# Kernel optimization log

Measured on AMD Instinct MI355X. Metric: run time of the kernel, lower is better.

## Reference

```python
import jax, jax.numpy as jnp
import numpy as np
from jax.scipy.special import logsumexp

B, N, V = 16, 25, 10000
WDIM, HDIM, ZDIM, SD = 512, 512, 64, 256
T, NT = 60, 30
S = NT + T          # all_states
NEG = -1e9          # log-zero surrogate (keeps grads finite)


def setup_inputs() -> dict:
    key = jax.random.key(0)
    ks = jax.random.split(key, 32)
    g = lambda k, shape, s=0.02: (jax.random.normal(k, shape) * s).astype(jnp.float32)
    z4 = lambda *shape: jnp.zeros(shape, jnp.float32)
    return {
        "x": jax.random.randint(ks[0], (B, N), 0, V),
        "eps": jax.random.normal(ks[1], (B, ZDIM), dtype=jnp.float32),
        "enc_emb": g(ks[2], (V, WDIM), 0.1),
        "lstm_f_wih": g(ks[3], (WDIM, 4 * HDIM)),
        "lstm_f_whh": g(ks[4], (HDIM, 4 * HDIM)),
        "lstm_f_b": z4(4 * HDIM),
        "lstm_b_wih": g(ks[5], (WDIM, 4 * HDIM)),
        "lstm_b_whh": g(ks[6], (HDIM, 4 * HDIM)),
        "lstm_b_b": z4(4 * HDIM),
        "encp_w": g(ks[7], (2 * HDIM, 2 * ZDIM)),
        "encp_b": z4(2 * ZDIM),
        "t_emb": g(ks[8], (T, SD), 1.0),
        "nt_emb": g(ks[9], (NT, SD), 1.0),
        "root_emb": g(ks[10], (1, SD), 1.0),
        "rule_w": g(ks[11], (SD + ZDIM, S * S)),
        "rule_b": z4(S * S),
        "root_w1": g(ks[12], (SD + ZDIM, SD)),
        "root_b1": z4(SD),
        "root_resw": g(ks[13], (4, SD, SD)),
        "root_resb": z4(4, SD),
        "root_w2": g(ks[14], (SD, NT)),
        "root_b2": z4(NT),
        "voc_w1": g(ks[15], (SD + ZDIM, SD)),
        "voc_b1": z4(SD),
        "voc_resw": g(ks[16], (4, SD, SD)),
        "voc_resb": z4(4, SD),
        "voc_w2": g(ks[17], (SD, V)),
        "voc_b2": z4(V),
    }


def _mlp(h0, w1, b1, resw, resb, w2, b2):
    h = h0 @ w1 + b1
    for i in range(2):
        a = jax.nn.relu(h @ resw[2 * i] + resb[2 * i])
        h = jax.nn.relu(a @ resw[2 * i + 1] + resb[2 * i + 1]) + h
    return h @ w2 + b2


def _lstm(emb_tbw, wih, whh, b):
    # emb_tbw: [time, batch, w_dim] -> hidden states [time, batch, H]
    H = whh.shape[0]
    Bsz = emb_tbw.shape[1]

    def step(carry, xt):
        h, c = carry
        gates = xt @ wih + h @ whh + b
        i, f, gg, o = jnp.split(gates, 4, axis=-1)
        c = jax.nn.sigmoid(f) * c + jax.nn.sigmoid(i) * jnp.tanh(gg)
        h = jax.nn.sigmoid(o) * jnp.tanh(c)
        return (h, c), h

    init = (jnp.zeros((Bsz, H), emb_tbw.dtype), jnp.zeros((Bsz, H), emb_tbw.dtype))
    _, hs = jax.lax.scan(step, init, emb_tbw)
    return hs


def _inside(unary, rule, root):
    # unary: [B,n,T] preterminal scores; rule: [B,NT,S,S]; root: [B,NT]
    Bsz, n, _ = unary.shape
    chart = jnp.full((Bsz, n, n, S), NEG, unary.dtype)
    ar = jnp.arange(n)
    chart = chart.at[:, ar, ar, NT:].set(unary)  # width-1 spans = terminals
    for w in range(2, n + 1):
        ii = jnp.arange(n - w + 1)          # span starts
        u = jnp.arange(1, w)                # split offsets
        left = chart[:, ii[:, None], ii[:, None] + u[None, :] - 1, :]    # [B,ns,w-1,S]
        right = chart[:, ii[:, None] + u[None, :], ii[:, None] + w - 1, :]
        # lse over split points, then over (B,C) children against rules
        m2 = logsumexp(left[..., :, None] + right[..., None, :], axis=2)  # [B,ns,S,S]
        score = logsumexp(rule[:, None] + m2[:, :, None], axis=(-2, -1))  # [B,ns,NT]
        chart = chart.at[:, ii, ii + w - 1, :NT].set(score)
    return logsumexp(root + chart[:, 0, n - 1, :NT], axis=-1)  # [B]


def reference(x, eps, enc_emb, lstm_f_wih, lstm_f_whh, lstm_f_b,
              lstm_b_wih, lstm_b_whh, lstm_b_b, encp_w, encp_b,
              t_emb, nt_emb, root_emb, rule_w, rule_b,
              root_w1, root_b1, root_resw, root_resb, root_w2, root_b2,
              voc_w1, voc_b1, voc_resw, voc_resb, voc_w2, voc_b2):
    # --- variational encoder ---
    emb_t = jnp.swapaxes(enc_emb[x], 0, 1)                      # [N,B,W]
    hf = _lstm(emb_t, lstm_f_wih, lstm_f_whh, lstm_f_b)
    hb = _lstm(emb_t[::-1], lstm_b_wih, lstm_b_whh, lstm_b_b)[::-1]
    h = jnp.concatenate([hf, hb], axis=-1).max(axis=0)          # [B,2H] max over time
    params = h @ encp_w + encp_b
    mean, logvar = params[:, :ZDIM], params[:, ZDIM:]
    kl = (-0.5 * (logvar - mean ** 2 - jnp.exp(logvar) + 1.0)).sum(1)
    z = jnp.exp(0.5 * logvar) * eps + mean                       # [B,z]
    # --- root scores ---
    root_in = jnp.concatenate([jnp.broadcast_to(root_emb, (B, SD)), z], 1)
    root_scores = jax.nn.log_softmax(
        _mlp(root_in, root_w1, root_b1, root_resw, root_resb, root_w2, root_b2), axis=1)
    # --- unary scores (score each preterminal once, gather per token) ---
    t_in = jnp.concatenate([jnp.broadcast_to(t_emb[None], (B, T, SD)),
                            jnp.broadcast_to(z[:, None], (B, T, ZDIM))], -1)
    vocab_scores = jax.nn.log_softmax(
        _mlp(t_in, voc_w1, voc_b1, voc_resw, voc_resb, voc_w2, voc_b2), axis=-1)  # [B,T,V]
    unary = vocab_scores[jnp.arange(B)[:, None], :, x]           # [B,N,T]
    # --- binary rule scores ---
    nt_in = jnp.concatenate([jnp.broadcast_to(nt_emb[None], (B, NT, SD)),
                             jnp.broadcast_to(z[:, None], (B, NT, ZDIM))], -1)
    rule_scores = jax.nn.log_softmax(nt_in @ rule_w + rule_b, axis=-1).reshape(B, NT, S, S)
    # --- inside algorithm ---
    log_Z = _inside(unary, rule_scores, root_scores)
    return -log_Z, kl
```

## Files before the change

### kernel.cpp

```cpp
#include <hip/hip_runtime.h>
#include <hip/hip_bf16.h>
#include <math.h>

#define BB 16
#define NN 25
#define VV 10000
#define WD 512
#define HD 512
#define ZD 64
#define SDIM 256
#define TT 60
#define NTS 30
#define SSYM 90
#define S2 8100
#define NEGV -1000000000.0f

__global__ void k_emb(const int* __restrict__ x, const float* __restrict__ enc_emb,
                      float* __restrict__ emb) {
    int i = blockIdx.x * 256 + threadIdx.x;
    if (i >= 400 * 512) return;
    int r = i >> 9, k = i & 511;
    emb[i] = enc_emb[(size_t)x[r] * 512 + k];
}

__global__ __launch_bounds__(256) void gemm_f32(const float* __restrict__ A,
    const float* __restrict__ Bm, const float* __restrict__ bias,
    const float* __restrict__ res, float* __restrict__ C,
    int M, int Nn, int K, int do_relu)
{
    __shared__ float As[16][65];
    __shared__ float Bs[16][65];
    int tid = threadIdx.x;
    int tx = tid & 15, ty = tid >> 4;
    int bm = blockIdx.y * 64, bn = blockIdx.x * 64;
    float acc[4][4] = {};
    for (int k0 = 0; k0 < K; k0 += 16) {
#pragma unroll
        for (int l = 0; l < 4; ++l) {
            int idx = tid * 4 + l;
            int kk = idx & 15, mm = idx >> 4;
            int gr = bm + mm;
            As[kk][mm] = (gr < M) ? A[(size_t)gr * K + (k0 + kk)] : 0.f;
            int kb = idx >> 6, nn = idx & 63;
            int gc = bn + nn;
            Bs[kb][nn] = (gc < Nn) ? Bm[(size_t)(k0 + kb) * Nn + gc] : 0.f;
        }
        __syncthreads();
#pragma unroll
        for (int kk = 0; kk < 16; ++kk) {
            float av[4], bv[4];
#pragma unroll
            for (int i = 0; i < 4; ++i) av[i] = As[kk][ty * 4 + i];
#pragma unroll
            for (int j = 0; j < 4; ++j) bv[j] = Bs[kk][tx * 4 + j];
#pragma unroll
            for (int i = 0; i < 4; ++i)
#pragma unroll
                for (int j = 0; j < 4; ++j) acc[i][j] += av[i] * bv[j];
        }
        __syncthreads();
    }
#pragma unroll
    for (int i = 0; i < 4; ++i) {
        int r = bm + ty * 4 + i;
        if (r >= M) continue;
#pragma unroll
        for (int j = 0; j < 4; ++j) {
            int cc = bn + tx * 4 + j;
            if (cc >= Nn) continue;
            float v = acc[i][j] + (bias ? bias[cc] : 0.f);
            if (do_relu) v = fmaxf(v, 0.f);
            if (res) v += res[(size_t)r * Nn + cc];
            C[(size_t)r * Nn + cc] = v;
        }
    }
}

__global__ void k_lstm_init(float* hbuf, float* cbuf, float* hmax) {
    int i = blockIdx.x * 256 + threadIdx.x;
    if (i < 32768) hbuf[i] = 0.f;
    if (i < 16384) cbuf[i] = 0.f;
    if (i < 16384) hmax[i] = -3.0e38f;
}

__global__ __launch_bounds__(256) void k_lstm_gates(const float* __restrict__ whh_f,
    const float* __restrict__ whh_b, const float* __restrict__ hbuf,
    float* __restrict__ gp, int t)
{
    int blk = blockIdx.x;
    int d = blk >> 6, kc = (blk >> 3) & 7, cb = blk & 7;
    const float* whh = d ? whh_b : whh_f;
    int pp = t & 1;
    const float* hp = hbuf + d * 16384 + pp * 8192;
    __shared__ float hs[16][64];
    for (int i = threadIdx.x; i < 1024; i += 256) {
        int b = i >> 6, k = i & 63;
        hs[b][k] = hp[b * 512 + kc * 64 + k];
    }
    __syncthreads();
    int col = cb * 256 + threadIdx.x;
    float acc[16];
#pragma unroll
    for (int b = 0; b < 16; ++b) acc[b] = 0.f;
    const float* wp = whh + (size_t)(kc * 64) * 2048 + col;
    for (int k = 0; k < 64; ++k) {
        float w = wp[(size_t)k * 2048];
#pragma unroll
        for (int b = 0; b < 16; ++b) acc[b] += w * hs[b][k];
    }
#pragma unroll
    for (int b = 0; b < 16; ++b)
        gp[((size_t)(d * 16 + b) * 2048 + col) * 8 + kc] = acc[b];
}

__global__ __launch_bounds__(256) void k_lstm_update(const float* __restrict__ xg_f,
    const float* __restrict__ xg_b, const float* __restrict__ gp,
    float* __restrict__ hbuf, float* __restrict__ cbuf, float* __restrict__ hmax, int t)
{
    int gid = blockIdx.x * 256 + threadIdx.x;
    int d = gid >> 13, r = gid & 8191;
    int b = r >> 9, m = r & 511;
    int tt = d ? (24 - t) : t;
    const float* xg = d ? xg_b : xg_f;
    const float* xr = xg + (size_t)(b * 25 + tt) * 2048;
    float g4[4];
#pragma unroll
    for (int q = 0; q < 4; ++q) {
        int col = q * 512 + m;
        float s = xr[col];
        const float* pp = gp + ((size_t)(d * 16 + b) * 2048 + col) * 8;
#pragma unroll
        for (int kc = 0; kc < 8; ++kc) s += pp[kc];
        g4[q] = s;
    }
    float si = 1.f / (1.f + expf(-g4[0]));
    float sf = 1.f / (1.f + expf(-g4[1]));
    float tg = tanhf(g4[2]);
    float so = 1.f / (1.f + expf(-g4[3]));
    float* c = cbuf + d * 8192;
    float cc = sf * c[r] + si * tg;
    float hh = so * tanhf(cc);
    c[r] = cc;
    hbuf[d * 16384 + ((t & 1) ^ 1) * 8192 + r] = hh;
    float* hm = hmax + b * 1024 + d * 512 + m;
    *hm = fmaxf(*hm, hh);
}

__global__ __launch_bounds__(128) void k_encoder(const float* __restrict__ hmax,
    const float* __restrict__ encp_w, const float* __restrict__ encp_b,
    const float* __restrict__ eps, float* __restrict__ z, float* __restrict__ outp)
{
    int b = blockIdx.x, j = threadIdx.x;
    __shared__ float hrow[1024];
    for (int i = j; i < 1024; i += 128) hrow[i] = hmax[b * 1024 + i];
    __syncthreads();
    float dot = encp_b[j];
    for (int k = 0; k < 1024; ++k) dot += hrow[k] * encp_w[(size_t)k * 128 + j];
    __shared__ float prm[128];
    prm[j] = dot;
    __syncthreads();
    __shared__ float red[64];
    if (j < 64) {
        float mean = prm[j], lv = prm[64 + j];
        z[b * 64 + j] = expf(0.5f * lv) * eps[b * 64 + j] + mean;
        red[j] = -0.5f * (lv - mean * mean - expf(lv) + 1.f);
    }
    __syncthreads();
    if (j == 0) {
        float s = 0.f;
        for (int q = 0; q < 64; ++q) s += red[q];
        outp[16 + b] = s;
    }
}

__global__ void k_tin(const float* __restrict__ t_emb, const float* __restrict__ z,
                      float* __restrict__ tin) {
    int i = blockIdx.x * 256 + threadIdx.x;
    if (i >= 960 * 320) return;
    int r = i / 320, k = i % 320;
    int b = r / 60, t = r % 60;
    tin[i] = (k < 256) ? t_emb[t * 256 + k] : z[b * 64 + (k - 256)];
}
__global__ void k_ntin(const float* __restrict__ nt_emb, const float* __restrict__ z,
                       float* __restrict__ ntin) {
    int i = blockIdx.x * 256 + threadIdx.x;
    if (i >= 480 * 320) return;
    int r = i / 320, k = i % 320;
    int b = r / 30, nt = r % 30;
    ntin[i] = (k < 256) ? nt_emb[nt * 256 + k] : z[b * 64 + (k - 256)];
}

__global__ __launch_bounds__(256) void k_vocab_final(const float* __restrict__ A,
    const float* __restrict__ Bm, const float* __restrict__ bias, const int* __restrict__ x,
    float* __restrict__ pmax, float* __restrict__ psum, float* __restrict__ unary)
{
    __shared__ float As[16][65];
    __shared__ float Bs[16][65];
    __shared__ int xs[400];
    int tid = threadIdx.x;
    for (int i = tid; i < 400; i += 256) xs[i] = x[i];
    int tx = tid & 15, ty = tid >> 4;
    int bm = blockIdx.y * 64, bn = blockIdx.x * 64;
    float acc[4][4] = {};
    for (int k0 = 0; k0 < 256; k0 += 16) {
#pragma unroll
        for (int l = 0; l < 4; ++l) {
            int idx = tid * 4 + l;
            int kk = idx & 15, mm = idx >> 4;
            As[kk][mm] = A[(size_t)(bm + mm) * 256 + k0 + kk];
            int kb = idx >> 6, nn = idx & 63;
            int gc = bn + nn;
            Bs[kb][nn] = (gc < VV) ? Bm[(size_t)(k0 + kb) * VV + gc] : 0.f;
        }
        __syncthreads();
#pragma unroll
        for (int kk = 0; kk < 16; ++kk) {
            float av[4], bv[4];
#pragma unroll
            for (int i = 0; i < 4; ++i) av[i] = As[kk][ty * 4 + i];
#pragma unroll
            for (int j = 0; j < 4; ++j) bv[j] = Bs[kk][tx * 4 + j];
#pragma unroll
            for (int i = 0; i < 4; ++i)
#pragma unroll
                for (int j = 0; j < 4; ++j) acc[i][j] += av[i] * bv[j];
        }
        __syncthreads();
    }
    __shared__ float rmax[64][17];
    __shared__ float rsum[64][17];
#pragma unroll
    for (int i = 0; i < 4; ++i) {
        int r = bm + ty * 4 + i;
        int b = r / 60, t = r % 60;
        float vv[4];
        float lm = -3.0e38f;
#pragma unroll
        for (int j = 0; j < 4; ++j) {
            int cc = bn + tx * 4 + j;
            if (cc < VV) { float v = acc[i][j] + bias[cc]; vv[j] = v; lm = fmaxf(lm, v); }
            else vv[j] = -3.0e38f;
        }
        float ls = 0.f;
#pragma unroll
        for (int j = 0; j < 4; ++j)
            if (bn + tx * 4 + j < VV) ls += expf(vv[j] - lm);
        rmax[ty * 4 + i][tx] = lm;
        rsum[ty * 4 + i][tx] = ls;
#pragma unroll
        for (int j = 0; j < 4; ++j) {
            int cc = bn + tx * 4 + j;
            if (cc < VV) {
                for (int n = 0; n < 25; ++n)
                    if (xs[b * 25 + n] == cc)
                        unary[((size_t)b * 25 + n) * 60 + t] = vv[j];
            }
        }
    }
    __syncthreads();
    if (tid < 64) {
        int row = tid;
        float m = -3.0e38f;
        for (int q = 0; q < 16; ++q) m = fmaxf(m, rmax[row][q]);
        float s = 0.f;
        for (int q = 0; q < 16; ++q) {
            float rm = rmax[row][q];
            if (rm > -1e38f) s += rsum[row][q] * expf(rm - m);
        }
        int r = bm + row;
        pmax[(size_t)r * 157 + blockIdx.x] = m;
        psum[(size_t)r * 157 + blockIdx.x] = s;
    }
}

__global__ void k_vlse(const float* __restrict__ pmax, const float* __restrict__ psum,
                       float* __restrict__ vlse) {
    int r = blockIdx.x * 256 + threadIdx.x;
    if (r >= 960) return;
    float m = -3.0e38f;
    for (int cb = 0; cb < 157; ++cb) m = fmaxf(m, pmax[(size_t)r * 157 + cb]);
    float s = 0.f;
    for (int cb = 0; cb < 157; ++cb) {
        float rm = pmax[(size_t)r * 157 + cb];
        if (rm > -1e38f) s += psum[(size_t)r * 157 + cb] * expf(rm - m);
    }
    vlse[r] = m + logf(s);
}

__global__ __launch_bounds__(256) void k_root(const float* __restrict__ root_emb,
    const float* __restrict__ z, const float* __restrict__ w1, const float* __restrict__ b1,
    const float* __restrict__ resw, const float* __restrict__ resb,
    const float* __restrict__ w2, const float* __restrict__ b2, float* __restrict__ rootlog)
{
    int b = blockIdx.x, j = threadIdx.x;
    __shared__ float h0[320];
    __shared__ float h[256], a[256];
    if (j < 256) h0[j] = root_emb[j];
    if (j < 64)  h0[256 + j] = z[b * 64 + j];
    __syncthreads();
    float d1 = b1[j];
    for (int k = 0; k < 320; ++k) d1 += h0[k] * w1[(size_t)k * 256 + j];
    h[j] = d1;
    for (int l = 0; l < 2; ++l) {
        __syncthreads();
        const float* rw0 = resw + (size_t)(2 * l) * 65536;
        const float* rw1 = resw + (size_t)(2 * l + 1) * 65536;
        float t1 = resb[2 * l * 256 + j];
        for (int k = 0; k < 256; ++k) t1 += h[k] * rw0[(size_t)k * 256 + j];
        a[j] = fmaxf(t1, 0.f);
        __syncthreads();
        float t2 = resb[(2 * l + 1) * 256 + j];
        for (int k = 0; k < 256; ++k) t2 += a[k] * rw1[(size_t)k * 256 + j];
        h[j] = fmaxf(t2, 0.f) + h[j];
    }
    __syncthreads();
    if (j < 30) {
        float d2 = b2[j];
        for (int k = 0; k < 256; ++k) d2 += h[k] * w2[(size_t)k * 30 + j];
        rootlog[b * 30 + j] = d2;
    }
}

__global__ __launch_bounds__(256) void k_rule_softmax(float* __restrict__ rl) {
    int r = blockIdx.x;
    float* row = rl + (size_t)r * S2;
    __shared__ float red[256];
    float m = -3.0e38f;
    for (int i = threadIdx.x; i < S2; i += 256) m = fmaxf(m, row[i]);
    red[threadIdx.x] = m; __syncthreads();
    for (int s = 128; s > 0; s >>= 1) {
        if (threadIdx.x < s) red[threadIdx.x] = fmaxf(red[threadIdx.x], red[threadIdx.x + s]);
        __syncthreads();
    }
    m = red[0];
    __syncthreads();
    float sum = 0.f;
    for (int i = threadIdx.x; i < S2; i += 256) sum += expf(row[i] - m);
    red[threadIdx.x] = sum; __syncthreads();
    for (int s = 128; s > 0; s >>= 1) {
        if (threadIdx.x < s) red[threadIdx.x] += red[threadIdx.x + s];
        __syncthreads();
    }
    float inv = 1.f / red[0];
    __syncthreads();
    for (int i = threadIdx.x; i < S2; i += 256) row[i] = expf(row[i] - m) * inv;
}

__global__ void k_chart_fill(float* __restrict__ chart) {
    int i = blockIdx.x * 256 + threadIdx.x;
    if (i < 900000) chart[i] = NEGV;
}
__global__ void k_chart_diag(const float* __restrict__ unary, const float* __restrict__ vlse,
                             float* __restrict__ chart) {
    int idx = blockIdx.x * 256 + threadIdx.x;
    if (idx >= 24000) return;
    int b = idx / 1500;
    int rem = idx % 1500;
    int n = rem / 60, t = rem % 60;
    chart[(((size_t)b * 25 + n) * 25 + n) * 90 + 30 + t] = unary[idx] - vlse[b * 60 + t];
}

__global__ __launch_bounds__(256) void k_inside_em(const float* __restrict__ chart,
    float* __restrict__ EM, float* __restrict__ m2max, int w)
{
    int i = blockIdx.x, b = blockIdx.y;
    int wm1 = w - 1;
    __shared__ float EL[24][91], ER[24][91];
    __shared__ float mlu[24], mru[24];
    __shared__ float Msh;
    int total = wm1 * 90;
    for (int idx = threadIdx.x; idx < total; idx += 256) {
        int u = idx / 90, s = idx % 90;
        EL[u][s] = chart[(((size_t)b * 25 + i) * 25 + (i + u)) * 90 + s];
        ER[u][s] = chart[(((size_t)b * 25 + (i + u + 1)) * 25 + (i + w - 1)) * 90 + s];
    }
    __syncthreads();
    if (threadIdx.x < wm1) {
        int u = threadIdx.x;
        float m = -3.0e38f;
        for (int s = 0; s < 90; ++s) m = fmaxf(m, EL[u][s]);
        mlu[u] = m;
    } else if (threadIdx.x >= 64 && threadIdx.x < 64 + wm1) {
        int u = threadIdx.x - 64;
        float m = -3.0e38f;
        for (int s = 0; s < 90; ++s) m = fmaxf(m, ER[u][s]);
        mru[u] = m;
    }
    __syncthreads();
    if (threadIdx.x == 0) {
        float M = -3.0e38f;
        for (int u = 0; u < wm1; ++u) M = fmaxf(M, mlu[u] + mru[u]);
        Msh = M;
    }
    __syncthreads();
    float M = Msh;
    for (int idx = threadIdx.x; idx < total; idx += 256) {
        int u = idx / 90, s = idx % 90;
        EL[u][s] = expf(EL[u][s] + mru[u] - M);
        ER[u][s] = expf(ER[u][s] - mru[u]);
    }
    __syncthreads();
    float* em = EM + ((size_t)b * 24 + i) * S2;
    for (int o = threadIdx.x; o < S2; o += 256) {
        int Bs = o / 90, Cs = o % 90;
        float acc = 0.f;
        for (int u = 0; u < wm1; ++u) acc += EL[u][Bs] * ER[u][Cs];
        em[o] = acc;
    }
    if (threadIdx.x == 0) m2max[b * 24 + i] = M;
}

__global__ __launch_bounds__(512) void k_inside_dot(const float* __restrict__ ER,
    const float* __restrict__ EM, float* __restrict__ dotp, int w)
{
    int kc = blockIdx.x, b = blockIdx.y;
    int npos = 26 - w;
    int L = S2 - kc * 256; if (L > 256) L = 256;
    __shared__ float ERs[30][257];
    __shared__ float EMs[24][257];
    for (int idx = threadIdx.x; idx < 30 * L; idx += 512) {
        int A = idx / L, l = idx % L;
        ERs[A][l] = ER[((size_t)b * 30 + A) * S2 + kc * 256 + l];
    }
    for (int idx = threadIdx.x; idx < npos * L; idx += 512) {
        int i = idx / L, l = idx % L;
        EMs[i][l] = EM[((size_t)b * 24 + i) * S2 + kc * 256 + l];
    }
    __syncthreads();
    for (int p = threadIdx.x; p < npos * 30; p += 512) {
        int i = p / 30, A = p % 30;
        float acc = 0.f;
        for (int l = 0; l < L; ++l) acc += EMs[i][l] * ERs[A][l];
        dotp[(((size_t)b * 24 + i) * 30 + A) * 32 + kc] = acc;
    }
}

__global__ void k_inside_score(const float* __restrict__ dotp, const float* __restrict__ m2max,
                               float* __restrict__ chart, int w)
{
    int npos = 26 - w;
    int tot = 16 * npos * 30;
    int p = blockIdx.x * 256 + threadIdx.x;
    if (p >= tot) return;
    int b = p / (npos * 30);
    int rem = p % (npos * 30);
    int i = rem / 30, A = rem % 30;
    const float* dp = dotp + (((size_t)b * 24 + i) * 30 + A) * 32;
    float s = 0.f;
#pragma unroll
    for (int kc = 0; kc < 32; ++kc) s += dp[kc];
    float v = m2max[b * 24 + i] + logf(fmaxf(s, 1e-38f));
    chart[(((size_t)b * 25 + i) * 25 + (i + w - 1)) * 90 + A] = v;
}

__global__ void k_final(const float* __restrict__ rootlog, const float* __restrict__ chart,
                        float* __restrict__ outp) {
    int b = threadIdx.x;
    if (b >= 16) return;
    const float* rl = rootlog + b * 30;
    const float* ch = chart + (((size_t)b * 25 + 0) * 25 + 24) * 90;
    float m1 = -3.0e38f, m2v = -3.0e38f;
    for (int A = 0; A < 30; ++A) {
        m1 = fmaxf(m1, rl[A]);
        m2v = fmaxf(m2v, rl[A] + ch[A]);
    }
    float s1 = 0.f, s2 = 0.f;
    for (int A = 0; A < 30; ++A) {
        s1 += expf(rl[A] - m1);
        s2 += expf(rl[A] + ch[A] - m2v);
    }
    outp[b] = -((m2v + logf(s2)) - (m1 + logf(s1)));
}

extern "C" void kernel_launch(void* const* d_in, const int* in_sizes, int n_in,
                              void* d_out, int out_size, void* d_ws, size_t ws_size,
                              hipStream_t stream)
{
    const int*   x        = (const int*)  d_in[0];
    const float* eps      = (const float*)d_in[1];
    const float* enc_emb  = (const float*)d_in[2];
    const float* f_wih    = (const float*)d_in[3];
    const float* f_whh    = (const float*)d_in[4];
    const float* f_bb     = (const float*)d_in[5];
    const float* b_wih    = (const float*)d_in[6];
    const float* b_whh    = (const float*)d_in[7];
    const float* b_bb     = (const float*)d_in[8];
    const float* encp_w   = (const float*)d_in[9];
    const float* encp_b   = (const float*)d_in[10];
    const float* t_emb    = (const float*)d_in[11];
    const float* nt_emb   = (const float*)d_in[12];
    const float* root_emb = (const float*)d_in[13];
    const float* rule_w   = (const float*)d_in[14];
    const float* rule_bi  = (const float*)d_in[15];
    const float* root_w1  = (const float*)d_in[16];
    const float* root_b1  = (const float*)d_in[17];
    const float* root_rw  = (const float*)d_in[18];
    const float* root_rb  = (const float*)d_in[19];
    const float* root_w2  = (const float*)d_in[20];
    const float* root_b2  = (const float*)d_in[21];
    const float* voc_w1   = (const float*)d_in[22];
    const float* voc_b1   = (const float*)d_in[23];
    const float* voc_rw   = (const float*)d_in[24];
    const float* voc_rb   = (const float*)d_in[25];
    const float* voc_w2   = (const float*)d_in[26];
    const float* voc_b2   = (const float*)d_in[27];
    float* out = (float*)d_out;

    float* Wp = (float*)d_ws;
    size_t o = 0;
    float* emb   = Wp + o; o += 400 * 512;
    float* xg_f  = Wp + o; o += 400 * 2048;
    float* xg_b  = Wp + o; o += 400 * 2048;
    float* hbuf  = Wp + o; o += 2 * 2 * 8192;
    float* cbuf  = Wp + o; o += 2 * 8192;
    float* hmax  = Wp + o; o += 16384;
    float* gp    = Wp + o; o += 2 * 16 * 2048 * 8;
    float* z     = Wp + o; o += 1024;
    float* tin   = Wp + o; o += 960 * 320;
    float* ntin  = Wp + o; o += 480 * 320;
    float* mlpH  = Wp + o; o += 960 * 256;
    float* mlpA  = Wp + o; o += 960 * 256;
    float* mlpH2 = Wp + o; o += 960 * 256;
    float* pmax  = Wp + o; o += 960 * 157;
    float* psum  = Wp + o; o += 960 * 157;
    float* vlse  = Wp + o; o += 960;
    float* unary = Wp + o; o += 24000;
    float* ruleB = Wp + o; o += 480 * S2;
    float* rootlog = Wp + o; o += 480;
    float* chart = Wp + o; o += 900000;
    float* EM    = Wp + o; o += 16 * 24 * S2;
    float* m2m   = Wp + o; o += 16 * 24;
    float* dotp  = Wp + o; o += 16 * 24 * 30 * 32;

    k_emb<<<800, 256, 0, stream>>>(x, enc_emb, emb);
    gemm_f32<<<dim3(32, 7), 256, 0, stream>>>(emb, f_wih, f_bb, nullptr, xg_f, 400, 2048, 512, 0);
    gemm_f32<<<dim3(32, 7), 256, 0, stream>>>(emb, b_wih, b_bb, nullptr, xg_b, 400, 2048, 512, 0);
    k_lstm_init<<<128, 256, 0, stream>>>(hbuf, cbuf, hmax);
    for (int t = 0; t < 25; ++t) {
        k_lstm_gates<<<128, 256, 0, stream>>>(f_whh, b_whh, hbuf, gp, t);
        k_lstm_update<<<64, 256, 0, stream>>>(xg_f, xg_b, gp, hbuf, cbuf, hmax, t);
    }
    k_encoder<<<16, 128, 0, stream>>>(hmax, encp_w, encp_b, eps, z, out);

    k_tin<<<1200, 256, 0, stream>>>(t_emb, z, tin);
    k_ntin<<<600, 256, 0, stream>>>(nt_emb, z, ntin);
    gemm_f32<<<dim3(4, 15), 256, 0, stream>>>(tin, voc_w1, voc_b1, nullptr, mlpH, 960, 256, 320, 0);
    gemm_f32<<<dim3(4, 15), 256, 0, stream>>>(mlpH, voc_rw, voc_rb, nullptr, mlpA, 960, 256, 256, 1);
    gemm_f32<<<dim3(4, 15), 256, 0, stream>>>(mlpA, voc_rw + 65536, voc_rb + 256, mlpH, mlpH2, 960, 256, 256, 1);
    gemm_f32<<<dim3(4, 15), 256, 0, stream>>>(mlpH2, voc_rw + 131072, voc_rb + 512, nullptr, mlpA, 960, 256, 256, 1);
    gemm_f32<<<dim3(4, 15), 256, 0, stream>>>(mlpA, voc_rw + 196608, voc_rb + 768, mlpH2, mlpH, 960, 256, 256, 1);
    k_vocab_final<<<dim3(157, 15), 256, 0, stream>>>(mlpH, voc_w2, voc_b2, x, pmax, psum, unary);
    k_vlse<<<4, 256, 0, stream>>>(pmax, psum, vlse);
    k_root<<<16, 256, 0, stream>>>(root_emb, z, root_w1, root_b1, root_rw, root_rb, root_w2, root_b2, rootlog);
    gemm_f32<<<dim3(127, 8), 256, 0, stream>>>(ntin, rule_w, rule_bi, nullptr, ruleB, 480, S2, 320, 0);
    k_rule_softmax<<<480, 256, 0, stream>>>(ruleB);

    k_chart_fill<<<(900000 + 255) / 256, 256, 0, stream>>>(chart);
    k_chart_diag<<<(24000 + 255) / 256, 256, 0, stream>>>(unary, vlse, chart);
    for (int w = 2; w <= 25; ++w) {
        int npos = 26 - w;
        k_inside_em<<<dim3(npos, 16), 256, 0, stream>>>(chart, EM, m2m, w);
        k_inside_dot<<<dim3(32, 16), 512, 0, stream>>>(ruleB, EM, dotp, w);
        int tot = 16 * npos * 30;
        k_inside_score<<<(tot + 255) / 256, 256, 0, stream>>>(dotp, m2m, chart, w);
    }
    k_final<<<1, 64, 0, stream>>>(rootlog, chart, out);
}
```

Before: 2.080 ms.

## Fuse inside-algorithm kernels per span and vectorize GEMM tile loads

Merges the three per-width inside kernels (outer-product EM, chunked dot with rule scores, score reduction) into one kernel. Each block keeps its EM matrix in shared memory and does wave-level dot products against the rule probabilities, writing the chart entry directly. This removes the EM, dotp and m2max global buffers and two launches per width. Separately, the SGEMM and vocab GEMM now use float4 global and shared-memory loads with padded rows. The catch is that each block re-reads the full 30x8100 rule slice per span, and there are fewer blocks for large widths.

```diff
diff --git a/kernel.cpp b/kernel.cpp
--- a/kernel.cpp
+++ b/kernel.cpp
@@ -28,35 +28,42 @@
     const float* __restrict__ res, float* __restrict__ C,
     int M, int Nn, int K, int do_relu)
 {
-    __shared__ float As[16][65];
-    __shared__ float Bs[16][65];
+    __shared__ float As[16][68];
+    __shared__ float Bs[16][68];
     int tid = threadIdx.x;
     int tx = tid & 15, ty = tid >> 4;
     int bm = blockIdx.y * 64, bn = blockIdx.x * 64;
+    int mm = tid >> 2, l4 = (tid & 3) * 4;
+    int kb = tid >> 4, nn = (tid & 15) * 4;
+    bool bfull = (bn + 64 <= Nn);
     float acc[4][4] = {};
     for (int k0 = 0; k0 < K; k0 += 16) {
-#pragma unroll
-        for (int l = 0; l < 4; ++l) {
-            int idx = tid * 4 + l;
-            int kk = idx & 15, mm = idx >> 4;
-            int gr = bm + mm;
-            As[kk][mm] = (gr < M) ? A[(size_t)gr * K + (k0 + kk)] : 0.f;
-            int kb = idx >> 6, nn = idx & 63;
-            int gc = bn + nn;
-            Bs[kb][nn] = (gc < Nn) ? Bm[(size_t)(k0 + kb) * Nn + gc] : 0.f;
-        }
+        float4 a4 = make_float4(0.f, 0.f, 0.f, 0.f);
+        if (bm + mm < M) a4 = *(const float4*)&A[(size_t)(bm + mm) * K + k0 + l4];
+        As[l4 + 0][mm] = a4.x; As[l4 + 1][mm] = a4.y;
+        As[l4 + 2][mm] = a4.z; As[l4 + 3][mm] = a4.w;
+        float4 b4;
+        if (bfull) {
+            b4 = *(const float4*)&Bm[(size_t)(k0 + kb) * Nn + bn + nn];
+        } else {
+            const float* br = &Bm[(size_t)(k0 + kb) * Nn];
+            b4.x = (bn + nn + 0 < Nn) ? br[bn + nn + 0] : 0.f;
+            b4.y = (bn + nn + 1 < Nn) ? br[bn + nn + 1] : 0.f;
+            b4.z = (bn + nn + 2 < Nn) ? br[bn + nn + 2] : 0.f;
+            b4.w = (bn + nn + 3 < Nn) ? br[bn + nn + 3] : 0.f;
+        }
+        *(float4*)&Bs[kb][nn] = b4;
         __syncthreads();
 #pragma unroll
         for (int kk = 0; kk < 16; ++kk) {
-            float av[4], bv[4];
-#pragma unroll
-            for (int i = 0; i < 4; ++i) av[i] = As[kk][ty * 4 + i];
-#pragma unroll
-            for (int j = 0; j < 4; ++j) bv[j] = Bs[kk][tx * 4 + j];
+            float4 av = *(const float4*)&As[kk][ty * 4];
+            float4 bv = *(const float4*)&Bs[kk][tx * 4];
+            float avf[4] = {av.x, av.y, av.z, av.w};
+            float bvf[4] = {bv.x, bv.y, bv.z, bv.w};
 #pragma unroll
             for (int i = 0; i < 4; ++i)
 #pragma unroll
-                for (int j = 0; j < 4; ++j) acc[i][j] += av[i] * bv[j];
+                for (int j = 0; j < 4; ++j) acc[i][j] += avf[i] * bvf[j];
         }
         __syncthreads();
     }
@@ -194,36 +201,43 @@
     const float* __restrict__ Bm, const float* __restrict__ bias, const int* __restrict__ x,
     float* __restrict__ pmax, float* __restrict__ psum, float* __restrict__ unary)
 {
-    __shared__ float As[16][65];
-    __shared__ float Bs[16][65];
+    __shared__ float As[16][68];
+    __shared__ float Bs[16][68];
     __shared__ int xs[400];
     int tid = threadIdx.x;
     for (int i = tid; i < 400; i += 256) xs[i] = x[i];
     int tx = tid & 15, ty = tid >> 4;
     int bm = blockIdx.y * 64, bn = blockIdx.x * 64;
+    int mm = tid >> 2, l4 = (tid & 3) * 4;
+    int kb = tid >> 4, nn = (tid & 15) * 4;
+    bool bfull = (bn + 64 <= VV);
     float acc[4][4] = {};
     for (int k0 = 0; k0 < 256; k0 += 16) {
-#pragma unroll
-        for (int l = 0; l < 4; ++l) {
-            int idx = tid * 4 + l;
-            int kk = idx & 15, mm = idx >> 4;
-            As[kk][mm] = A[(size_t)(bm + mm) * 256 + k0 + kk];
-            int kb = idx >> 6, nn = idx & 63;
-            int gc = bn + nn;
-            Bs[kb][nn] = (gc < VV) ? Bm[(size_t)(k0 + kb) * VV + gc] : 0.f;
-        }
+        float4 a4 = *(const float4*)&A[(size_t)(bm + mm) * 256 + k0 + l4];
+        As[l4 + 0][mm] = a4.x; As[l4 + 1][mm] = a4.y;
+        As[l4 + 2][mm] = a4.z; As[l4 + 3][mm] = a4.w;
+        float4 b4;
+        if (bfull) {
+            b4 = *(const float4*)&Bm[(size_t)(k0 + kb) * VV + bn + nn];
+        } else {
+            const float* br = &Bm[(size_t)(k0 + kb) * VV];
+            b4.x = (bn + nn + 0 < VV) ? br[bn + nn + 0] : 0.f;
+            b4.y = (bn + nn + 1 < VV) ? br[bn + nn + 1] : 0.f;
+            b4.z = (bn + nn + 2 < VV) ? br[bn + nn + 2] : 0.f;
+            b4.w = (bn + nn + 3 < VV) ? br[bn + nn + 3] : 0.f;
+        }
+        *(float4*)&Bs[kb][nn] = b4;
         __syncthreads();
 #pragma unroll
         for (int kk = 0; kk < 16; ++kk) {
-            float av[4], bv[4];
-#pragma unroll
-            for (int i = 0; i < 4; ++i) av[i] = As[kk][ty * 4 + i];
-#pragma unroll
-            for (int j = 0; j < 4; ++j) bv[j] = Bs[kk][tx * 4 + j];
+            float4 av = *(const float4*)&As[kk][ty * 4];
+            float4 bv = *(const float4*)&Bs[kk][tx * 4];
+            float avf[4] = {av.x, av.y, av.z, av.w};
+            float bvf[4] = {bv.x, bv.y, bv.z, bv.w};
 #pragma unroll
             for (int i = 0; i < 4; ++i)
 #pragma unroll
-                for (int j = 0; j < 4; ++j) acc[i][j] += av[i] * bv[j];
+                for (int j = 0; j < 4; ++j) acc[i][j] += avf[i] * bvf[j];
         }
         __syncthreads();
     }
@@ -360,12 +374,13 @@
     chart[(((size_t)b * 25 + n) * 25 + n) * 90 + 30 + t] = unary[idx] - vlse[b * 60 + t];
 }
 
-__global__ __launch_bounds__(256) void k_inside_em(const float* __restrict__ chart,
-    float* __restrict__ EM, float* __restrict__ m2max, int w)
+__global__ __launch_bounds__(256) void k_inside_fused(const float* __restrict__ ruleB,
+    float* __restrict__ chart, int w)
 {
     int i = blockIdx.x, b = blockIdx.y;
     int wm1 = w - 1;
     __shared__ float EL[24][91], ER[24][91];
+    __shared__ float EMs[S2];
     __shared__ float mlu[24], mru[24];
     __shared__ float Msh;
     int total = wm1 * 90;
@@ -400,57 +415,24 @@
         ER[u][s] = expf(ER[u][s] - mru[u]);
     }
     __syncthreads();
-    float* em = EM + ((size_t)b * 24 + i) * S2;
     for (int o = threadIdx.x; o < S2; o += 256) {
-        int Bs = o / 90, Cs = o % 90;
+        int Bs_ = o / 90, Cs = o % 90;
         float acc = 0.f;
-        for (int u = 0; u < wm1; ++u) acc += EL[u][Bs] * ER[u][Cs];
-        em[o] = acc;
-    }
-    if (threadIdx.x == 0) m2max[b * 24 + i] = M;
-}
-
-__global__ __launch_bounds__(512) void k_inside_dot(const float* __restrict__ ER,
-    const float* __restrict__ EM, float* __restrict__ dotp, int w)
-{
-    int kc = blockIdx.x, b = blockIdx.y;
-    int npos = 26 - w;
-    int L = S2 - kc * 256; if (L > 256) L = 256;
-    __shared__ float ERs[30][257];
-    __shared__ float EMs[24][257];
-    for (int idx = threadIdx.x; idx < 30 * L; idx += 512) {
-        int A = idx / L, l = idx % L;
-        ERs[A][l] = ER[((size_t)b * 30 + A) * S2 + kc * 256 + l];
-    }
-    for (int idx = threadIdx.x; idx < npos * L; idx += 512) {
-        int i = idx / L, l = idx % L;
-        EMs[i][l] = EM[((size_t)b * 24 + i) * S2 + kc * 256 + l];
-    }
-    __syncthreads();
-    for (int p = threadIdx.x; p < npos * 30; p += 512) {
-        int i = p / 30, A = p % 30;
+        for (int u = 0; u < wm1; ++u) acc += EL[u][Bs_] * ER[u][Cs];
+        EMs[o] = acc;
+    }
+    __syncthreads();
+    int wv = threadIdx.x >> 6, lane = threadIdx.x & 63;
+    for (int A = wv; A < 30; A += 4) {
+        const float* rb = ruleB + ((size_t)b * 30 + A) * S2;
         float acc = 0.f;
-        for (int l = 0; l < L; ++l) acc += EMs[i][l] * ERs[A][l];
-        dotp[(((size_t)b * 24 + i) * 30 + A) * 32 + kc] = acc;
-    }
-}
-
-__global__ void k_inside_score(const float* __restrict__ dotp, const float* __restrict__ m2max,
-                               float* __restrict__ chart, int w)
-{
-    int npos = 26 - w;
-    int tot = 16 * npos * 30;
-    int p = blockIdx.x * 256 + threadIdx.x;
-    if (p >= tot) return;
-    int b = p / (npos * 30);
-    int rem = p % (npos * 30);
-    int i = rem / 30, A = rem % 30;
-    const float* dp = dotp + (((size_t)b * 24 + i) * 30 + A) * 32;
-    float s = 0.f;
-#pragma unroll
-    for (int kc = 0; kc < 32; ++kc) s += dp[kc];
-    float v = m2max[b * 24 + i] + logf(fmaxf(s, 1e-38f));
-    chart[(((size_t)b * 25 + i) * 25 + (i + w - 1)) * 90 + A] = v;
+        for (int l = lane; l < S2; l += 64) acc += EMs[l] * rb[l];
+#pragma unroll
+        for (int off = 32; off > 0; off >>= 1) acc += __shfl_down(acc, off);
+        if (lane == 0)
+            chart[(((size_t)b * 25 + i) * 25 + (i + w - 1)) * 90 + A] =
+                M + logf(fmaxf(acc, 1e-38f));
+    }
 }
 
 __global__ void k_final(const float* __restrict__ rootlog, const float* __restrict__ chart,
@@ -528,9 +510,6 @@
     float* ruleB = Wp + o; o += 480 * S2;
     float* rootlog = Wp + o; o += 480;
     float* chart = Wp + o; o += 900000;
-    float* EM    = Wp + o; o += 16 * 24 * S2;
-    float* m2m   = Wp + o; o += 16 * 24;
-    float* dotp  = Wp + o; o += 16 * 24 * 30 * 32;
 
     k_emb<<<800, 256, 0, stream>>>(x, enc_emb, emb);
     gemm_f32<<<dim3(32, 7), 256, 0, stream>>>(emb, f_wih, f_bb, nullptr, xg_f, 400, 2048, 512, 0);
@@ -559,10 +538,7 @@
     k_chart_diag<<<(24000 + 255) / 256, 256, 0, stream>>>(unary, vlse, chart);
     for (int w = 2; w <= 25; ++w) {
         int npos = 26 - w;
-        k_inside_em<<<dim3(npos, 16), 256, 0, stream>>>(chart, EM, m2m, w);
-        k_inside_dot<<<dim3(32, 16), 512, 0, stream>>>(ruleB, EM, dotp, w);
-        int tot = 16 * npos * 30;
-        k_inside_score<<<(tot + 255) / 256, 256, 0, stream>>>(dotp, m2m, chart, w);
+        k_inside_fused<<<dim3(npos, 16), 256, 0, stream>>>(ruleB, chart, w);
     }
     k_final<<<1, 64, 0, stream>>>(rootlog, chart, out);
 }
```

New measurement: 7.500 ms. 3.61x slower.
